# Optimization experiments

Measured on AMD Instinct MI355X. Metric: run time of the kernel, lower is better.

The kernel has to match this reference:

```python
import jax, jax.numpy as jnp
import numpy as np

N_RAYS, N_SAMPLES, GRID, APP_DIM, FEATC = 2048, 256, 128, 27, 128
VIEWPE, FEAPE = 2, 2
NEAR, FAR = 2.0, 6.0
AABB0, AABB1 = -1.5, 1.5
DENSITY_SHIFT, DISTANCE_SCALE = -10.0, 25.0
IN_MLPC = 2 * VIEWPE * 3 + 2 * FEAPE * APP_DIM + 3 + APP_DIM  # 150


def positional_encoding(x, freqs):
    fb = (2.0 ** jnp.arange(freqs)).astype(x.dtype)
    p = (x[..., None] * fb).reshape(x.shape[:-1] + (freqs * x.shape[-1],))
    return jnp.concatenate([jnp.sin(p), jnp.cos(p)], axis=-1)


def trilinear(vol, coords):
    # vol: [C, D, H, W]; coords: [P, 3] in [-1, 1] ordered (x, y, z) like torch grid_sample (align_corners=True)
    C, D, H, W = vol.shape
    x = (coords[:, 0] + 1.0) * 0.5 * (W - 1)
    y = (coords[:, 1] + 1.0) * 0.5 * (H - 1)
    z = (coords[:, 2] + 1.0) * 0.5 * (D - 1)
    x0 = jnp.clip(jnp.floor(x), 0, W - 2).astype(jnp.int32)
    y0 = jnp.clip(jnp.floor(y), 0, H - 2).astype(jnp.int32)
    z0 = jnp.clip(jnp.floor(z), 0, D - 2).astype(jnp.int32)
    x1, y1, z1 = x0 + 1, y0 + 1, z0 + 1
    fx, fy, fz = x - x0, y - y0, z - z0
    g = lambda zi, yi, xi: vol[:, zi, yi, xi]  # [C, P]
    out = (g(z0, y0, x0) * ((1 - fz) * (1 - fy) * (1 - fx))
           + g(z0, y0, x1) * ((1 - fz) * (1 - fy) * fx)
           + g(z0, y1, x0) * ((1 - fz) * fy * (1 - fx))
           + g(z0, y1, x1) * ((1 - fz) * fy * fx)
           + g(z1, y0, x0) * (fz * (1 - fy) * (1 - fx))
           + g(z1, y0, x1) * (fz * (1 - fy) * fx)
           + g(z1, y1, x0) * (fz * fy * (1 - fx))
           + g(z1, y1, x1) * (fz * fy * fx))
    return out  # [C, P]


def setup_inputs() -> dict:
    key = jax.random.key(0)
    ks = jax.random.split(key, 10)
    return {
        'rays_o': jax.random.uniform(ks[0], (N_RAYS, 3), jnp.float32, -0.5, 0.5) + jnp.array([0.0, 0.0, -4.0]),
        'rays_d': jax.random.normal(ks[1], (N_RAYS, 3), jnp.float32) * 0.1 + jnp.array([0.0, 0.0, 1.0]),
        'density_volume': jax.random.normal(ks[2], (1, GRID, GRID, GRID), jnp.float32) * 2.0 + 10.0,
        'app_volume': jax.random.normal(ks[3], (APP_DIM, GRID, GRID, GRID), jnp.float32) * 0.1,
        'w1': jax.random.normal(ks[4], (IN_MLPC, FEATC), jnp.float32) * 0.05,
        'b1': jnp.zeros((FEATC,), jnp.float32),
        'w2': jax.random.normal(ks[5], (FEATC, FEATC), jnp.float32) * 0.05,
        'b2': jnp.zeros((FEATC,), jnp.float32),
        'w3': jax.random.normal(ks[6], (FEATC, 3), jnp.float32) * 0.05,
        'b3': jnp.zeros((3,), jnp.float32),
    }


def reference(rays_o, rays_d, density_volume, app_volume, w1, b1, w2, b2, w3, b3):
    viewdirs = rays_d / jnp.linalg.norm(rays_d, axis=-1, keepdims=True)  # [N, 3]
    z_vals = jnp.linspace(NEAR, FAR, N_SAMPLES, dtype=rays_o.dtype)      # [S]
    z_vals = jnp.broadcast_to(z_vals, (N_RAYS, N_SAMPLES))
    pts = rays_o[:, None, :] + viewdirs[:, None, :] * z_vals[..., None]  # [N, S, 3]
    dists = jnp.concatenate([z_vals[:, 1:] - z_vals[:, :-1], z_vals[:, -1:] * 0 + (FAR - NEAR) / (N_SAMPLES - 1)], axis=-1)

    # normalize_coord: (xyz - aabb0) * (2 / aabbSize) - 1
    coords = jnp.clip((pts - AABB0) * (2.0 / (AABB1 - AABB0)) - 1.0, -1.0, 1.0).reshape(-1, 3)

    # density lookup + feature2density (softplus with shift)
    sigma_feat = trilinear(density_volume, coords)[0].reshape(N_RAYS, N_SAMPLES)
    sigma = jax.nn.softplus(sigma_feat + DENSITY_SHIFT)

    # raw2alpha: alpha, cumprod transmittance, weights
    alpha = 1.0 - jnp.exp(-sigma * dists * DISTANCE_SCALE)               # [N, S]
    T = jnp.cumprod(jnp.concatenate([jnp.ones((N_RAYS, 1), alpha.dtype), 1.0 - alpha + 1e-10], axis=-1), axis=-1)
    weights = alpha * T[:, :-1]                                          # [N, S]

    # MLPRender_Fea shading on all sampled points
    feat = trilinear(app_volume, coords).T                               # [P, app_dim]
    vd = jnp.broadcast_to(viewdirs[:, None, :], (N_RAYS, N_SAMPLES, 3)).reshape(-1, 3)
    mlp_in = jnp.concatenate([feat, vd, positional_encoding(feat, FEAPE), positional_encoding(vd, VIEWPE)], axis=-1)
    h = jax.nn.relu(mlp_in @ w1 + b1)
    h = jax.nn.relu(h @ w2 + b2)
    rgb = jax.nn.sigmoid(h @ w3 + b3).reshape(N_RAYS, N_SAMPLES, 3)

    acc_map = jnp.sum(weights, axis=-1)                                  # [N]
    rgb_map = jnp.sum(weights[..., None] * rgb, axis=-2)                 # [N, 3]
    rgb_map = jnp.clip(rgb_map + (1.0 - acc_map)[..., None], 0.0, 1.0)   # white background
    return rgb_map
```

## Files before the change

kernel.cpp:

```cpp
#include <hip/hip_runtime.h>
#include <math.h>
#include <limits.h>

#define N_RAYS 2048
#define NSAMP  256
#define NPTS   (N_RAYS * NSAMP)
#define NCHUNK (NPTS / 64)
#define GRIDN  128
#define G2     (GRIDN * GRIDN)
#define G3     (GRIDN * GRIDN * GRIDN)
#define APPC   27
#define CHP    28
#define FEATC  128
#define K1PAD  160
#define ASTR   168
#define HSTR   136
#define H2STR  130

typedef __attribute__((ext_vector_type(8))) short short8;
typedef __attribute__((ext_vector_type(4))) float float4v;

__device__ __forceinline__ unsigned short f2bf(float f) {
  unsigned int u = __float_as_uint(f);
  return (unsigned short)((u + 0x7FFFu + ((u >> 16) & 1u)) >> 16);
}
__device__ __forceinline__ float bf2f(unsigned short u) {
  return __uint_as_float(((unsigned int)u) << 16);
}

__device__ __forceinline__ void grid_coords(float cx, float cy, float cz,
                                            int& x0, int& y0, int& z0,
                                            float& fx, float& fy, float& fz) {
  float x = (cx + 1.0f) * 0.5f * 127.0f;
  float y = (cy + 1.0f) * 0.5f * 127.0f;
  float z = (cz + 1.0f) * 0.5f * 127.0f;
  float x0f = fminf(fmaxf(floorf(x), 0.0f), 126.0f);
  float y0f = fminf(fmaxf(floorf(y), 0.0f), 126.0f);
  float z0f = fminf(fmaxf(floorf(z), 0.0f), 126.0f);
  x0 = (int)x0f; y0 = (int)y0f; z0 = (int)z0f;
  fx = x - x0f; fy = y - y0f; fz = z - z0f;
}

__global__ __launch_bounds__(256)
void dvol_transpose(const float* __restrict__ dvol, float* __restrict__ dvolT) {
  __shared__ float tile[32][33];
  int y  = blockIdx.x & 127;
  int zt = ((blockIdx.x >> 7) & 3) * 32;
  int xt = (blockIdx.x >> 9) * 32;
  int tx = threadIdx.x & 31;
  int r0 = threadIdx.x >> 5;
  #pragma unroll
  for (int i = 0; i < 4; ++i) {
    int zr = r0 + i * 8;
    tile[zr][tx] = dvol[((zt + zr) * GRIDN + y) * GRIDN + xt + tx];
  }
  __syncthreads();
  #pragma unroll
  for (int i = 0; i < 4; ++i) {
    int xr = r0 + i * 8;
    dvolT[((xt + xr) * GRIDN + y) * GRIDN + zt + tx] = tile[tx][xr];
  }
}

template <bool TRANS>
__global__ __launch_bounds__(256)
void ray_kernel(const float* __restrict__ rays_o, const float* __restrict__ rays_d,
                const float* __restrict__ dvol,
                float* __restrict__ weights_ws, float* __restrict__ acc_ws,
                int* __restrict__ live_flags, int* __restrict__ block_bounds) {
  int r = blockIdx.x, s = threadIdx.x;
  int lane = s & 63, wv = s >> 6;
  float ox = rays_o[r*3+0], oy = rays_o[r*3+1], oz = rays_o[r*3+2];
  float dx = rays_d[r*3+0], dy = rays_d[r*3+1], dz = rays_d[r*3+2];
  float inv = rsqrtf(dx*dx + dy*dy + dz*dz);
  dx *= inv; dy *= inv; dz *= inv;
  float z = 2.0f + (4.0f / 255.0f) * (float)s;
  float px = ox + dx * z, py = oy + dy * z, pz = oz + dz * z;
  float cx = fminf(fmaxf((px + 1.5f) * (2.0f/3.0f) - 1.0f, -1.0f), 1.0f);
  float cy = fminf(fmaxf((py + 1.5f) * (2.0f/3.0f) - 1.0f, -1.0f), 1.0f);
  float cz = fminf(fmaxf((pz + 1.5f) * (2.0f/3.0f) - 1.0f, -1.0f), 1.0f);
  int x0, y0, z0; float fx, fy, fz;
  grid_coords(cx, cy, cz, x0, y0, z0, fx, fy, fz);
  float gx = 1.0f - fx, gy = 1.0f - fy, gz = 1.0f - fz;
  float sf;
  if (TRANS) {
    int base = (x0 * GRIDN + y0) * GRIDN + z0;
    float v000 = dvol[base],            v001 = dvol[base + 1];
    float v010 = dvol[base + GRIDN],    v011 = dvol[base + GRIDN + 1];
    float v100 = dvol[base + G2],       v101 = dvol[base + G2 + 1];
    float v110 = dvol[base + G2+GRIDN], v111 = dvol[base + G2+GRIDN+1];
    float c00 = gz * v000 + fz * v001;
    float c01 = gz * v010 + fz * v011;
    float c10 = gz * v100 + fz * v101;
    float c11 = gz * v110 + fz * v111;
    sf = gx * (gy * c00 + fy * c01) + fx * (gy * c10 + fy * c11);
  } else {
    int base = (z0 * GRIDN + y0) * GRIDN + x0;
    sf = dvol[base]            * (gz*gy*gx) + dvol[base + 1]            * (gz*gy*fx)
       + dvol[base + GRIDN]    * (gz*fy*gx) + dvol[base + GRIDN + 1]    * (gz*fy*fx)
       + dvol[base + G2]       * (fz*gy*gx) + dvol[base + G2 + 1]       * (fz*gy*fx)
       + dvol[base + G2+GRIDN] * (fz*fy*gx) + dvol[base + G2+GRIDN+1]   * (fz*fy*fx);
  }
  float xv = sf - 10.0f;
  float sp = fmaxf(xv, 0.0f) + __logf(1.0f + __expf(-fabsf(xv)));
  float alpha = 1.0f - __expf(-sp * (100.0f / 255.0f));

  float tt = 1.0f - alpha + 1e-10f;
  float p = tt;
  #pragma unroll
  for (int d = 1; d < 64; d <<= 1) {
    float v = __shfl_up(p, d);
    if (lane >= d) p *= v;
  }
  __shared__ float wtot[4], wacc[4];
  __shared__ int s_mn[4][3], s_mx[4][3], s_live[4];
  if (lane == 63) wtot[wv] = p;
  __syncthreads();
  float pref = 1.0f;
  #pragma unroll
  for (int w2i = 0; w2i < 3; ++w2i) if (w2i < wv) pref *= wtot[w2i];
  float ex = __shfl_up(p, 1);
  if (lane == 0) ex = 1.0f;
  float T = pref * ex;
  float wgt = alpha * T;
  weights_ws[r * NSAMP + s] = wgt;

  float sum = wgt;
  #pragma unroll
  for (int d = 32; d; d >>= 1) sum += __shfl_xor(sum, d);
  int xa = __shfl(x0, 0), xb = __shfl(x0, 63);
  int ya = __shfl(y0, 0), yb = __shfl(y0, 63);
  int za = __shfl(z0, 0), zb = __shfl(z0, 63);
  if (lane == 0) {
    wacc[wv] = sum;
    int live = (sum >= 1e-5f) ? 1 : 0;
    live_flags[r * 4 + wv] = live;
    s_live[wv] = live;
    s_mn[wv][0] = min(xa, xb); s_mx[wv][0] = max(xa, xb);
    s_mn[wv][1] = min(ya, yb); s_mx[wv][1] = max(ya, yb);
    s_mn[wv][2] = min(za, zb); s_mx[wv][2] = max(za, zb);
  }
  __syncthreads();
  if (s == 0) {
    acc_ws[r] = wacc[0] + wacc[1] + wacc[2] + wacc[3];
    int mn[3] = {INT_MAX, INT_MAX, INT_MAX};
    int mx[3] = {-1, -1, -1};
    #pragma unroll
    for (int w = 0; w < 4; ++w) {
      if (s_live[w]) {
        #pragma unroll
        for (int i = 0; i < 3; ++i) {
          mn[i] = min(mn[i], s_mn[w][i]);
          mx[i] = max(mx[i], s_mx[w][i]);
        }
      }
    }
    block_bounds[r*6+0] = mn[0]; block_bounds[r*6+1] = mn[1]; block_bounds[r*6+2] = mn[2];
    block_bounds[r*6+3] = mx[0] + 1; block_bounds[r*6+4] = mx[1] + 1; block_bounds[r*6+5] = mx[2] + 1;
  }
}

__global__ __launch_bounds__(256)
void compact_kernel(const int* __restrict__ live_flags, const int* __restrict__ block_bounds,
                    int* __restrict__ count, int* __restrict__ worklist,
                    int* __restrict__ bounds) {
  int t = threadIdx.x;
  int id = blockIdx.x * 256 + t;
  int lane = t & 63, wv = t >> 6;
  int flag = live_flags[id];
  unsigned long long m = __ballot(flag != 0);
  int prefix = __popcll(m & ((1ull << lane) - 1ull));
  int wcount = __popcll(m);
  __shared__ int wbase[4];
  if (lane == 0) wbase[wv] = wcount;
  __syncthreads();
  if (t == 0) {
    int tot = wbase[0] + wbase[1] + wbase[2] + wbase[3];
    int base = atomicAdd(count, tot);
    #pragma unroll
    for (int w = 0; w < 4; ++w) { int c = wbase[w]; wbase[w] = base; base += c; }
  }
  __syncthreads();
  if (flag) worklist[wbase[wv] + prefix] = id;

  if (t < 64) {
    int rr = blockIdx.x * 64 + t;
    int mn0 = block_bounds[rr*6+0], mn1 = block_bounds[rr*6+1], mn2 = block_bounds[rr*6+2];
    int mx0 = block_bounds[rr*6+3], mx1 = block_bounds[rr*6+4], mx2 = block_bounds[rr*6+5];
    #pragma unroll
    for (int d = 32; d; d >>= 1) {
      mn0 = min(mn0, __shfl_xor(mn0, d)); mx0 = max(mx0, __shfl_xor(mx0, d));
      mn1 = min(mn1, __shfl_xor(mn1, d)); mx1 = max(mx1, __shfl_xor(mx1, d));
      mn2 = min(mn2, __shfl_xor(mn2, d)); mx2 = max(mx2, __shfl_xor(mx2, d));
    }
    if (t == 0) {
      atomicMin(&bounds[0], mn0); atomicMax(&bounds[3], mx0);
      atomicMin(&bounds[1], mn1); atomicMax(&bounds[4], mx1);
      atomicMin(&bounds[2], mn2); atomicMax(&bounds[5], mx2);
    }
  }
}

__global__ __launch_bounds__(256)
void transpose_kernel(const float* __restrict__ avol, unsigned short* __restrict__ appT,
                      const int* __restrict__ bounds) {
  int vblk = blockIdx.x * 512;
  int zb = vblk >> 14;
  int yb = (vblk & 16383) >> 7;
  int zmin = bounds[2], zmax = bounds[5];
  int ymin = bounds[1], ymax = bounds[4];
  if (zb < zmin || zb > zmax) return;
  if (yb + 3 < ymin || yb > ymax) return;
  int v0 = vblk + threadIdx.x * 2;
  int y = (v0 & 16383) >> 7;
  int x = v0 & 127;
  if (y < ymin || y > ymax) return;
  int xmin = bounds[0], xmax = bounds[3];
  if (x + 1 < xmin || x > xmax) return;

  float2 v[APPC];
  #pragma unroll
  for (int c = 0; c < APPC; ++c) v[c] = *(const float2*)&avol[(size_t)c * G3 + v0];
  unsigned short* dst = appT + (size_t)v0 * CHP;
  #pragma unroll
  for (int i = 0; i < 7; ++i) {
    ushort4 o;
    o.x = f2bf(v[4*i+0].x); o.y = f2bf(v[4*i+1].x);
    o.z = (4*i+2 < APPC) ? f2bf(v[4*i+2].x) : (unsigned short)0;
    o.w = (4*i+3 < APPC) ? f2bf(v[4*i+3].x) : (unsigned short)0;
    *(ushort4*)&dst[4*i] = o;
  }
  #pragma unroll
  for (int i = 0; i < 7; ++i) {
    ushort4 o;
    o.x = f2bf(v[4*i+0].y); o.y = f2bf(v[4*i+1].y);
    o.z = (4*i+2 < APPC) ? f2bf(v[4*i+2].y) : (unsigned short)0;
    o.w = (4*i+3 < APPC) ? f2bf(v[4*i+3].y) : (unsigned short)0;
    *(ushort4*)&dst[CHP + 4*i] = o;
  }
}

__global__ __launch_bounds__(256)
void prep_weights(const float* __restrict__ w1, const float* __restrict__ w2,
                  unsigned short* __restrict__ w1T, unsigned short* __restrict__ w2T) {
  int t = blockIdx.x * 256 + threadIdx.x;
  if (t < 128 * K1PAD) {
    int n = t / K1PAD, k = t - n * K1PAD;
    w1T[t] = (k < 150) ? f2bf(w1[k * 128 + n]) : (unsigned short)0;
  } else {
    int i = t - 128 * K1PAD;
    if (i < 128 * 128) {
      int n = i >> 7, k = i & 127;
      w2T[i] = f2bf(w2[k * 128 + n]);
    }
  }
}

template <bool USET>
__global__ __launch_bounds__(256)
void shade_kernel(const float* __restrict__ rays_o, const float* __restrict__ rays_d,
                  const float* __restrict__ avol, const unsigned short* __restrict__ appT,
                  const unsigned short* __restrict__ w1T, const unsigned short* __restrict__ w2T,
                  const float* __restrict__ b1, const float* __restrict__ b2,
                  const float* __restrict__ w3, const float* __restrict__ b3,
                  const float* __restrict__ weights_ws, float* __restrict__ rgb_accum,
                  const int* __restrict__ count, int* __restrict__ work_ctr,
                  const int* __restrict__ worklist) {
  __shared__ unsigned short A_lds[64 * ASTR];
  __shared__ unsigned short h1_lds[64 * HSTR];
  __shared__ int s_idx, s_n;

  int t = threadIdx.x;
  int lane = t & 63, wv = t >> 6;

  if (t == 0) s_n = *count;

  for (;;) {
    __syncthreads();
    if (t == 0) s_idx = atomicAdd(work_ctr, 1);
    __syncthreads();
    if (s_idx >= s_n) break;
    int chunk = worklist[s_idx];
    int gp0 = chunk * 64;
    int r = gp0 >> 8;

    {
      int q = t & 3, pt = t >> 2;
      int gp = gp0 + pt, s = gp & 255;
      float ox = rays_o[r*3+0], oy = rays_o[r*3+1], oz = rays_o[r*3+2];
      float dx = rays_d[r*3+0], dy = rays_d[r*3+1], dz = rays_d[r*3+2];
      float inv = rsqrtf(dx*dx + dy*dy + dz*dz);
      dx *= inv; dy *= inv; dz *= inv;
      float z = 2.0f + (4.0f / 255.0f) * (float)s;
      float px = ox + dx * z, py = oy + dy * z, pz = oz + dz * z;
      float cx = fminf(fmaxf((px + 1.5f) * (2.0f/3.0f) - 1.0f, -1.0f), 1.0f);
      float cy = fminf(fmaxf((py + 1.5f) * (2.0f/3.0f) - 1.0f, -1.0f), 1.0f);
      float cz = fminf(fmaxf((pz + 1.5f) * (2.0f/3.0f) - 1.0f, -1.0f), 1.0f);
      int x0, y0, z0; float fxg, fyg, fzg;
      grid_coords(cx, cy, cz, x0, y0, z0, fxg, fyg, fzg);
      float gxg = 1.0f - fxg, gyg = 1.0f - fyg, gzg = 1.0f - fzg;
      float w8[8];
      w8[0] = gzg*gyg*gxg; w8[1] = gzg*gyg*fxg;
      w8[2] = gzg*fyg*gxg; w8[3] = gzg*fyg*fxg;
      w8[4] = fzg*gyg*gxg; w8[5] = fzg*gyg*fxg;
      w8[6] = fzg*fyg*gxg; w8[7] = fzg*fyg*fxg;
      int ibase = (z0 * GRIDN + y0) * GRIDN + x0;

      int vi = ibase + (q >> 1) * G2 + (q & 1) * GRIDN;
      float wA = w8[2*q], wB = w8[2*q+1];
      float part[27];
      if (USET) {
        const ushort4* c0 = (const ushort4*)(appT + (size_t)vi * CHP);
        const ushort4* c1 = (const ushort4*)(appT + (size_t)(vi + 1) * CHP);
        ushort4 a[7], b[7];
        #pragma unroll
        for (int i = 0; i < 7; ++i) { a[i] = c0[i]; b[i] = c1[i]; }
        #pragma unroll
        for (int c = 0; c < 27; ++c) {
          unsigned short ua = (&a[c >> 2].x)[c & 3];
          unsigned short ub = (&b[c >> 2].x)[c & 3];
          part[c] = wA * bf2f(ua) + wB * bf2f(ub);
        }
      } else {
        #pragma unroll
        for (int c = 0; c < 27; ++c) {
          const float* base = avol + (size_t)c * G3 + vi;
          part[c] = wA * base[0] + wB * base[1];
        }
      }
      #pragma unroll
      for (int c = 0; c < 27; ++c) {
        float v = part[c];
        v += __shfl_xor(v, 1);
        v += __shfl_xor(v, 2);
        part[c] = v;
      }
      float f[7];
      #pragma unroll
      for (int j = 0; j < 7; ++j) {
        float vlo = (q & 1) ? part[7 + j] : part[j];
        float vhi = (q & 1) ? part[(21 + j < 27) ? 21 + j : 26] : part[14 + j];
        f[j] = (q & 2) ? vhi : vlo;
      }
      unsigned short* Arow = A_lds + pt * ASTR;
      int cbase = 7 * q;
      #pragma unroll
      for (int j = 0; j < 7; ++j) {
        int c = cbase + j;
        if (c < 27) {
          float fv = f[j];
          Arow[c] = f2bf(fv);
          float s1 = __sinf(fv),      c1 = __cosf(fv);
          float s2 = __sinf(2.0f*fv), c2 = __cosf(2.0f*fv);
          Arow[30 + 2*c] = f2bf(s1); Arow[31 + 2*c] = f2bf(s2);
          Arow[84 + 2*c] = f2bf(c1); Arow[85 + 2*c] = f2bf(c2);
        }
      }
      if (q == 3) {
        float vd[3] = {dx, dy, dz};
        #pragma unroll
        for (int d = 0; d < 3; ++d) {
          Arow[27 + d] = f2bf(vd[d]);
          float s1 = __sinf(vd[d]),      c1 = __cosf(vd[d]);
          float s2 = __sinf(2.0f*vd[d]), c2 = __cosf(2.0f*vd[d]);
          Arow[138 + 2*d] = f2bf(s1); Arow[139 + 2*d] = f2bf(s2);
          Arow[144 + 2*d] = f2bf(c1); Arow[145 + 2*d] = f2bf(c2);
        }
      }
      if (q == 1) {
        #pragma unroll
        for (int i = 0; i < 5; ++i) *(unsigned int*)&Arow[150 + 2*i] = 0u;
      }
    }
    __syncthreads();

    int nlo = lane & 15;
    int koff = (lane >> 4) * 8;
    int mrow = wv * 16 + nlo;

    short8 a1[5];
    #pragma unroll
    for (int kt = 0; kt < 5; ++kt)
      a1[kt] = *(const short8*)&A_lds[mrow * ASTR + kt * 32 + koff];
    #pragma unroll
    for (int nt = 0; nt < 8; ++nt) {
      float4v acc = {0.f, 0.f, 0.f, 0.f};
      #pragma unroll
      for (int kt = 0; kt < 5; ++kt) {
        short8 b = *(const short8*)&w1T[(nt * 16 + nlo) * K1PAD + kt * 32 + koff];
        acc = __builtin_amdgcn_mfma_f32_16x16x32_bf16(a1[kt], b, acc, 0, 0, 0);
      }
      float bv = b1[nt * 16 + nlo];
      #pragma unroll
      for (int rg = 0; rg < 4; ++rg) {
        int m = wv * 16 + (lane >> 4) * 4 + rg;
        float hv = fmaxf(acc[rg] + bv, 0.0f);
        h1_lds[m * HSTR + nt * 16 + nlo] = f2bf(hv);
      }
    }
    __syncthreads();

    short8 a2[4];
    #pragma unroll
    for (int kt = 0; kt < 4; ++kt)
      a2[kt] = *(const short8*)&h1_lds[mrow * HSTR + kt * 32 + koff];
    unsigned short* h2 = A_lds;
    #pragma unroll
    for (int nt = 0; nt < 8; ++nt) {
      float4v acc = {0.f, 0.f, 0.f, 0.f};
      #pragma unroll
      for (int kt = 0; kt < 4; ++kt) {
        short8 b = *(const short8*)&w2T[(nt * 16 + nlo) * FEATC + kt * 32 + koff];
        acc = __builtin_amdgcn_mfma_f32_16x16x32_bf16(a2[kt], b, acc, 0, 0, 0);
      }
      float bv = b2[nt * 16 + nlo];
      #pragma unroll
      for (int rg = 0; rg < 4; ++rg) {
        int m = wv * 16 + (lane >> 4) * 4 + rg;
        float hv = fmaxf(acc[rg] + bv, 0.0f);
        h2[m * H2STR + nt * 16 + nlo] = f2bf(hv);
      }
    }
    __syncthreads();

    if (wv < 3) {
      int j = wv, pp = lane;
      const unsigned short* h2row = h2 + pp * H2STR;
      float sum = b3[j];
      #pragma unroll
      for (int k = 0; k < FEATC; k += 4) {
        ushort4 hv = *(const ushort4*)&h2row[k];
        sum += bf2f(hv.x) * w3[(k+0)*3 + j] + bf2f(hv.y) * w3[(k+1)*3 + j]
             + bf2f(hv.z) * w3[(k+2)*3 + j] + bf2f(hv.w) * w3[(k+3)*3 + j];
      }
      float val = (1.0f / (1.0f + __expf(-sum))) * weights_ws[gp0 + pp];
      #pragma unroll
      for (int d = 32; d; d >>= 1) val += __shfl_xor(val, d);
      if (pp == 0) atomicAdd(&rgb_accum[r * 3 + j], val);
    }
  }
}

__global__ void finish_kernel(const float* __restrict__ rgb_accum,
                              const float* __restrict__ acc_ws,
                              float* __restrict__ out) {
  int i = blockIdx.x * blockDim.x + threadIdx.x;
  if (i < N_RAYS * 3) {
    int r = i / 3;
    float v = rgb_accum[i] + 1.0f - acc_ws[r];
    out[i] = fminf(fmaxf(v, 0.0f), 1.0f);
  }
}

extern "C" void kernel_launch(void* const* d_in, const int* in_sizes, int n_in,
                              void* d_out, int out_size, void* d_ws, size_t ws_size,
                              hipStream_t stream) {
  const float* rays_o = (const float*)d_in[0];
  const float* rays_d = (const float*)d_in[1];
  const float* dvol   = (const float*)d_in[2];
  const float* avol   = (const float*)d_in[3];
  const float* w1     = (const float*)d_in[4];
  const float* b1     = (const float*)d_in[5];
  const float* w2     = (const float*)d_in[6];
  const float* b2     = (const float*)d_in[7];
  const float* w3     = (const float*)d_in[8];
  const float* b3     = (const float*)d_in[9];
  float* out = (float*)d_out;

  float* weights_ws = (float*)d_ws;
  float* acc_ws     = weights_ws + NPTS;
  float* rgb_accum  = acc_ws + N_RAYS;
  int*   count      = (int*)(rgb_accum + N_RAYS * 3);
  int*   work_ctr   = count + 1;
  int*   bounds     = work_ctr + 1;
  int*   worklist   = bounds + 6;
  int*   live_flags = worklist + NCHUNK;
  int*   block_bounds = live_flags + NCHUNK;
  unsigned short* w1T = (unsigned short*)(block_bounds + N_RAYS * 6);
  unsigned short* w2T = w1T + 128 * K1PAD;
  float* dvolT = (float*)(w2T + 128 * 128);
  unsigned short* appT = (unsigned short*)(dvolT + G3);

  size_t fixed_bytes = (size_t)(NPTS + N_RAYS + N_RAYS * 3 + 8 + 2 * NCHUNK + N_RAYS * 6) * 4
                     + (size_t)(128 * K1PAD + 128 * 128) * 2;
  bool usedt = ws_size >= fixed_bytes + (size_t)G3 * 4;
  bool uset  = ws_size >= fixed_bytes + (size_t)G3 * 4 + (size_t)G3 * CHP * 2;

  hipMemsetAsync(rgb_accum, 0, (N_RAYS * 3 + 2) * sizeof(float), stream);
  hipMemsetAsync(bounds, 0x7f, 3 * sizeof(int), stream);
  hipMemsetAsync(bounds + 3, 0, 3 * sizeof(int), stream);
  prep_weights<<<(128 * K1PAD + 128 * 128 + 255) / 256, 256, 0, stream>>>(w1, w2, w1T, w2T);
  if (usedt) {
    dvol_transpose<<<2048, 256, 0, stream>>>(dvol, dvolT);
    ray_kernel<true><<<N_RAYS, 256, 0, stream>>>(rays_o, rays_d, dvolT, weights_ws, acc_ws,
                                                 live_flags, block_bounds);
  } else {
    ray_kernel<false><<<N_RAYS, 256, 0, stream>>>(rays_o, rays_d, dvol, weights_ws, acc_ws,
                                                  live_flags, block_bounds);
  }
  compact_kernel<<<NCHUNK / 256, 256, 0, stream>>>(live_flags, block_bounds,
                                                   count, worklist, bounds);
  if (uset) {
    transpose_kernel<<<G3 / 512, 256, 0, stream>>>(avol, appT, bounds);
    shade_kernel<true><<<1024, 256, 0, stream>>>(rays_o, rays_d, avol, appT, w1T, w2T,
                                                 b1, b2, w3, b3, weights_ws, rgb_accum,
                                                 count, work_ctr, worklist);
  } else {
    shade_kernel<false><<<1024, 256, 0, stream>>>(rays_o, rays_d, avol, appT, w1T, w2T,
                                                  b1, b2, w3, b3, weights_ws, rgb_accum,
                                                  count, work_ctr, worklist);
  }
  finish_kernel<<<(N_RAYS * 3 + 255) / 256, 256, 0, stream>>>(rgb_accum, acc_ws, out);
}
```

Before: 466.8 us.

## Compact shading work per sample by weight threshold instead of per 64-sample chunk

Shading work is now compacted per sample rather than per 64-sample chunk. The ray kernel ballots samples whose weight exceeds a small threshold, and a single-block scan plus a scatter kernel build a dense list of live sample ids. The shade kernel then processes only those samples and writes per-point rgb without atomics, and the finish kernel reduces them per ray. This is meant to skip MLP work on negligible-weight samples inside live chunks, at the cost of extra launches, gather indirection and an approximation that drops contributions below the threshold.

```diff
diff --git a/kernel.cpp b/kernel.cpp
--- a/kernel.cpp
+++ b/kernel.cpp
@@ -5,7 +5,6 @@
 #define N_RAYS 2048
 #define NSAMP  256
 #define NPTS   (N_RAYS * NSAMP)
-#define NCHUNK (NPTS / 64)
 #define GRIDN  128
 #define G2     (GRIDN * GRIDN)
 #define G3     (GRIDN * GRIDN * GRIDN)
@@ -16,6 +15,7 @@
 #define ASTR   168
 #define HSTR   136
 #define H2STR  130
+#define WTH    1e-7f
 
 typedef __attribute__((ext_vector_type(8))) short short8;
 typedef __attribute__((ext_vector_type(4))) float float4v;
@@ -67,7 +67,8 @@
 void ray_kernel(const float* __restrict__ rays_o, const float* __restrict__ rays_d,
                 const float* __restrict__ dvol,
                 float* __restrict__ weights_ws, float* __restrict__ acc_ws,
-                int* __restrict__ live_flags, int* __restrict__ block_bounds) {
+                unsigned long long* __restrict__ ray_mask, int* __restrict__ ray_count,
+                int* __restrict__ block_bounds) {
   int r = blockIdx.x, s = threadIdx.x;
   int lane = s & 63, wv = s >> 6;
   float ox = rays_o[r*3+0], oy = rays_o[r*3+1], oz = rays_o[r*3+2];
@@ -113,7 +114,7 @@
     if (lane >= d) p *= v;
   }
   __shared__ float wtot[4], wacc[4];
-  __shared__ int s_mn[4][3], s_mx[4][3], s_live[4];
+  __shared__ int s_cnt[4], s_mn[4][3], s_mx[4][3], s_live[4];
   if (lane == 63) wtot[wv] = p;
   __syncthreads();
   float pref = 1.0f;
@@ -128,14 +129,16 @@
   float sum = wgt;
   #pragma unroll
   for (int d = 32; d; d >>= 1) sum += __shfl_xor(sum, d);
+
+  unsigned long long m = __ballot(wgt >= WTH);
   int xa = __shfl(x0, 0), xb = __shfl(x0, 63);
   int ya = __shfl(y0, 0), yb = __shfl(y0, 63);
   int za = __shfl(z0, 0), zb = __shfl(z0, 63);
   if (lane == 0) {
     wacc[wv] = sum;
-    int live = (sum >= 1e-5f) ? 1 : 0;
-    live_flags[r * 4 + wv] = live;
-    s_live[wv] = live;
+    ray_mask[r * 4 + wv] = m;
+    s_cnt[wv] = __popcll(m);
+    s_live[wv] = (m != 0ull) ? 1 : 0;
     s_mn[wv][0] = min(xa, xb); s_mx[wv][0] = max(xa, xb);
     s_mn[wv][1] = min(ya, yb); s_mx[wv][1] = max(ya, yb);
     s_mn[wv][2] = min(za, zb); s_mx[wv][2] = max(za, zb);
@@ -143,6 +146,7 @@
   __syncthreads();
   if (s == 0) {
     acc_ws[r] = wacc[0] + wacc[1] + wacc[2] + wacc[3];
+    ray_count[r] = s_cnt[0] + s_cnt[1] + s_cnt[2] + s_cnt[3];
     int mn[3] = {INT_MAX, INT_MAX, INT_MAX};
     int mx[3] = {-1, -1, -1};
     #pragma unroll
@@ -161,43 +165,77 @@
 }
 
 __global__ __launch_bounds__(256)
-void compact_kernel(const int* __restrict__ live_flags, const int* __restrict__ block_bounds,
-                    int* __restrict__ count, int* __restrict__ worklist,
-                    int* __restrict__ bounds) {
-  int t = threadIdx.x;
-  int id = blockIdx.x * 256 + t;
-  int lane = t & 63, wv = t >> 6;
-  int flag = live_flags[id];
-  unsigned long long m = __ballot(flag != 0);
-  int prefix = __popcll(m & ((1ull << lane) - 1ull));
-  int wcount = __popcll(m);
-  __shared__ int wbase[4];
-  if (lane == 0) wbase[wv] = wcount;
+void scan_kernel(const int* __restrict__ ray_count, const int* __restrict__ block_bounds,
+                 int* __restrict__ ray_base, int* __restrict__ count,
+                 int* __restrict__ work_ctr, int* __restrict__ bounds) {
+  int t = threadIdx.x, lane = t & 63, wv = t >> 6;
+  int c[8], tsum = 0;
+  #pragma unroll
+  for (int j = 0; j < 8; ++j) { c[j] = ray_count[t*8+j]; tsum += c[j]; }
+  int p = tsum;
+  #pragma unroll
+  for (int d = 1; d < 64; d <<= 1) { int v = __shfl_up(p, d); if (lane >= d) p += v; }
+  __shared__ int wsum[4];
+  if (lane == 63) wsum[wv] = p;
+  __syncthreads();
+  int pref = 0;
+  #pragma unroll
+  for (int w = 0; w < 3; ++w) if (w < wv) pref += wsum[w];
+  int excl = pref + p - tsum;
+  #pragma unroll
+  for (int j = 0; j < 8; ++j) { ray_base[t*8+j] = excl; excl += c[j]; }
+  if (t == 255) { count[0] = excl; work_ctr[0] = 0; }
+
+  int mn0 = INT_MAX, mn1 = INT_MAX, mn2 = INT_MAX, mx0 = -1, mx1 = -1, mx2 = -1;
+  #pragma unroll
+  for (int j = 0; j < 8; ++j) {
+    int r = t*8+j;
+    if (c[j] > 0) {
+      mn0 = min(mn0, block_bounds[r*6+0]); mx0 = max(mx0, block_bounds[r*6+3]);
+      mn1 = min(mn1, block_bounds[r*6+1]); mx1 = max(mx1, block_bounds[r*6+4]);
+      mn2 = min(mn2, block_bounds[r*6+2]); mx2 = max(mx2, block_bounds[r*6+5]);
+    }
+  }
+  #pragma unroll
+  for (int d = 32; d; d >>= 1) {
+    mn0 = min(mn0, __shfl_xor(mn0, d)); mx0 = max(mx0, __shfl_xor(mx0, d));
+    mn1 = min(mn1, __shfl_xor(mn1, d)); mx1 = max(mx1, __shfl_xor(mx1, d));
+    mn2 = min(mn2, __shfl_xor(mn2, d)); mx2 = max(mx2, __shfl_xor(mx2, d));
+  }
+  __shared__ int bmn[4][3], bmx[4][3];
+  if (lane == 0) {
+    bmn[wv][0] = mn0; bmn[wv][1] = mn1; bmn[wv][2] = mn2;
+    bmx[wv][0] = mx0; bmx[wv][1] = mx1; bmx[wv][2] = mx2;
+  }
   __syncthreads();
   if (t == 0) {
-    int tot = wbase[0] + wbase[1] + wbase[2] + wbase[3];
-    int base = atomicAdd(count, tot);
     #pragma unroll
-    for (int w = 0; w < 4; ++w) { int c = wbase[w]; wbase[w] = base; base += c; }
-  }
-  __syncthreads();
-  if (flag) worklist[wbase[wv] + prefix] = id;
-
-  if (t < 64) {
-    int rr = blockIdx.x * 64 + t;
-    int mn0 = block_bounds[rr*6+0], mn1 = block_bounds[rr*6+1], mn2 = block_bounds[rr*6+2];
-    int mx0 = block_bounds[rr*6+3], mx1 = block_bounds[rr*6+4], mx2 = block_bounds[rr*6+5];
-    #pragma unroll
-    for (int d = 32; d; d >>= 1) {
-      mn0 = min(mn0, __shfl_xor(mn0, d)); mx0 = max(mx0, __shfl_xor(mx0, d));
-      mn1 = min(mn1, __shfl_xor(mn1, d)); mx1 = max(mx1, __shfl_xor(mx1, d));
-      mn2 = min(mn2, __shfl_xor(mn2, d)); mx2 = max(mx2, __shfl_xor(mx2, d));
-    }
-    if (t == 0) {
-      atomicMin(&bounds[0], mn0); atomicMax(&bounds[3], mx0);
-      atomicMin(&bounds[1], mn1); atomicMax(&bounds[4], mx1);
-      atomicMin(&bounds[2], mn2); atomicMax(&bounds[5], mx2);
-    }
+    for (int w = 1; w < 4; ++w) {
+      #pragma unroll
+      for (int i = 0; i < 3; ++i) {
+        bmn[0][i] = min(bmn[0][i], bmn[w][i]);
+        bmx[0][i] = max(bmx[0][i], bmx[w][i]);
+      }
+    }
+    bounds[0] = bmn[0][0]; bounds[1] = bmn[0][1]; bounds[2] = bmn[0][2];
+    bounds[3] = bmx[0][0]; bounds[4] = bmx[0][1]; bounds[5] = bmx[0][2];
+  }
+}
+
+__global__ __launch_bounds__(256)
+void scatter_kernel(const unsigned long long* __restrict__ ray_mask,
+                    const int* __restrict__ ray_base, int* __restrict__ sample_list) {
+  int t = threadIdx.x, lane = t & 63, wv = t >> 6;
+  int r = blockIdx.x * 4 + wv;
+  int base = ray_base[r];
+  int off = 0;
+  #pragma unroll
+  for (int w = 0; w < 4; ++w) {
+    unsigned long long m = ray_mask[r * 4 + w];
+    int flag = (int)((m >> lane) & 1ull);
+    int pre = __popcll(m & ((1ull << lane) - 1ull));
+    if (flag) sample_list[base + off + pre] = r * 256 + w * 64 + lane;
+    off += __popcll(m);
   }
 }
 
@@ -263,30 +301,33 @@
                   const unsigned short* __restrict__ w1T, const unsigned short* __restrict__ w2T,
                   const float* __restrict__ b1, const float* __restrict__ b2,
                   const float* __restrict__ w3, const float* __restrict__ b3,
-                  const float* __restrict__ weights_ws, float* __restrict__ rgb_accum,
+                  const float* __restrict__ weights_ws, float* __restrict__ rgb_pts,
                   const int* __restrict__ count, int* __restrict__ work_ctr,
-                  const int* __restrict__ worklist) {
+                  const int* __restrict__ sample_list) {
   __shared__ unsigned short A_lds[64 * ASTR];
   __shared__ unsigned short h1_lds[64 * HSTR];
-  __shared__ int s_idx, s_n;
+  __shared__ float wlds[64];
+  __shared__ int s_idx, s_items, s_n;
 
   int t = threadIdx.x;
   int lane = t & 63, wv = t >> 6;
 
-  if (t == 0) s_n = *count;
+  if (t == 0) { s_n = *count; s_items = (s_n + 63) >> 6; }
 
   for (;;) {
     __syncthreads();
     if (t == 0) s_idx = atomicAdd(work_ctr, 1);
     __syncthreads();
-    if (s_idx >= s_n) break;
-    int chunk = worklist[s_idx];
-    int gp0 = chunk * 64;
-    int r = gp0 >> 8;
+    if (s_idx >= s_items) break;
+    int base64 = s_idx * 64;
+    int n = s_n;
 
     {
       int q = t & 3, pt = t >> 2;
-      int gp = gp0 + pt, s = gp & 255;
+      int i = base64 + pt;
+      int id = (i < n) ? sample_list[i] : -1;
+      int sid = max(id, 0);
+      int r = sid >> 8, s = sid & 255;
       float ox = rays_o[r*3+0], oy = rays_o[r*3+1], oz = rays_o[r*3+2];
       float dx = rays_d[r*3+0], dy = rays_d[r*3+1], dz = rays_d[r*3+2];
       float inv = rsqrtf(dx*dx + dy*dy + dz*dz);
@@ -306,6 +347,8 @@
       w8[6] = fzg*fyg*gxg; w8[7] = fzg*fyg*fxg;
       int ibase = (z0 * GRIDN + y0) * GRIDN + x0;
 
+      if (q == 0) wlds[pt] = (id >= 0) ? weights_ws[sid] : 0.0f;
+
       int vi = ibase + (q >> 1) * G2 + (q & 1) * GRIDN;
       float wA = w8[2*q], wB = w8[2*q+1];
       float part[27];
@@ -314,7 +357,7 @@
         const ushort4* c1 = (const ushort4*)(appT + (size_t)(vi + 1) * CHP);
         ushort4 a[7], b[7];
         #pragma unroll
-        for (int i = 0; i < 7; ++i) { a[i] = c0[i]; b[i] = c1[i]; }
+        for (int i2 = 0; i2 < 7; ++i2) { a[i2] = c0[i2]; b[i2] = c1[i2]; }
         #pragma unroll
         for (int c = 0; c < 27; ++c) {
           unsigned short ua = (&a[c >> 2].x)[c & 3];
@@ -324,8 +367,8 @@
       } else {
         #pragma unroll
         for (int c = 0; c < 27; ++c) {
-          const float* base = avol + (size_t)c * G3 + vi;
-          part[c] = wA * base[0] + wB * base[1];
+          const float* bptr = avol + (size_t)c * G3 + vi;
+          part[c] = wA * bptr[0] + wB * bptr[1];
         }
       }
       #pragma unroll
@@ -369,7 +412,7 @@
       }
       if (q == 1) {
         #pragma unroll
-        for (int i = 0; i < 5; ++i) *(unsigned int*)&Arow[150 + 2*i] = 0u;
+        for (int i2 = 0; i2 < 5; ++i2) *(unsigned int*)&Arow[150 + 2*i2] = 0u;
       }
     }
     __syncthreads();
@@ -433,22 +476,33 @@
         sum += bf2f(hv.x) * w3[(k+0)*3 + j] + bf2f(hv.y) * w3[(k+1)*3 + j]
              + bf2f(hv.z) * w3[(k+2)*3 + j] + bf2f(hv.w) * w3[(k+3)*3 + j];
       }
-      float val = (1.0f / (1.0f + __expf(-sum))) * weights_ws[gp0 + pp];
-      #pragma unroll
-      for (int d = 32; d; d >>= 1) val += __shfl_xor(val, d);
-      if (pp == 0) atomicAdd(&rgb_accum[r * 3 + j], val);
-    }
-  }
-}
-
-__global__ void finish_kernel(const float* __restrict__ rgb_accum,
-                              const float* __restrict__ acc_ws,
-                              float* __restrict__ out) {
-  int i = blockIdx.x * blockDim.x + threadIdx.x;
-  if (i < N_RAYS * 3) {
-    int r = i / 3;
-    float v = rgb_accum[i] + 1.0f - acc_ws[r];
-    out[i] = fminf(fmaxf(v, 0.0f), 1.0f);
+      float val = (1.0f / (1.0f + __expf(-sum))) * wlds[pp];
+      rgb_pts[(size_t)(base64 + pp) * 4 + j] = val;
+    }
+  }
+}
+
+__global__ __launch_bounds__(256)
+void finish_kernel(const float* __restrict__ rgb_pts, const int* __restrict__ ray_base,
+                   const int* __restrict__ ray_count, const float* __restrict__ acc_ws,
+                   float* __restrict__ out) {
+  int t = threadIdx.x, lane = t & 63, wv = t >> 6;
+  int r = blockIdx.x * 4 + wv;
+  int base = ray_base[r], cnt = ray_count[r];
+  float s0 = 0.f, s1 = 0.f, s2 = 0.f;
+  for (int i = lane; i < cnt; i += 64) {
+    const float4 v = *(const float4*)&rgb_pts[(size_t)(base + i) * 4];
+    s0 += v.x; s1 += v.y; s2 += v.z;
+  }
+  #pragma unroll
+  for (int d = 32; d; d >>= 1) {
+    s0 += __shfl_xor(s0, d); s1 += __shfl_xor(s1, d); s2 += __shfl_xor(s2, d);
+  }
+  if (lane == 0) {
+    float a = 1.0f - acc_ws[r];
+    out[r*3+0] = fminf(fmaxf(s0 + a, 0.0f), 1.0f);
+    out[r*3+1] = fminf(fmaxf(s1 + a, 0.0f), 1.0f);
+    out[r*3+2] = fminf(fmaxf(s2 + a, 0.0f), 1.0f);
   }
 }
 
@@ -469,46 +523,47 @@
 
   float* weights_ws = (float*)d_ws;
   float* acc_ws     = weights_ws + NPTS;
-  float* rgb_accum  = acc_ws + N_RAYS;
-  int*   count      = (int*)(rgb_accum + N_RAYS * 3);
+  float* rgb_pts    = acc_ws + N_RAYS;
+  int*   count      = (int*)(rgb_pts + (size_t)(NPTS + 64) * 4);
   int*   work_ctr   = count + 1;
   int*   bounds     = work_ctr + 1;
-  int*   worklist   = bounds + 6;
-  int*   live_flags = worklist + NCHUNK;
-  int*   block_bounds = live_flags + NCHUNK;
-  unsigned short* w1T = (unsigned short*)(block_bounds + N_RAYS * 6);
+  int*   ray_count  = bounds + 6;
+  int*   ray_base   = ray_count + N_RAYS;
+  int*   block_bounds = ray_base + N_RAYS;
+  int*   sample_list  = block_bounds + N_RAYS * 6;
+  unsigned long long* ray_mask = (unsigned long long*)(sample_list + NPTS + 64);
+  unsigned short* w1T = (unsigned short*)(ray_mask + N_RAYS * 4);
   unsigned short* w2T = w1T + 128 * K1PAD;
   float* dvolT = (float*)(w2T + 128 * 128);
   unsigned short* appT = (unsigned short*)(dvolT + G3);
 
-  size_t fixed_bytes = (size_t)(NPTS + N_RAYS + N_RAYS * 3 + 8 + 2 * NCHUNK + N_RAYS * 6) * 4
+  size_t fixed_bytes = ((size_t)NPTS + N_RAYS + (size_t)(NPTS + 64) * 4
+                        + 8 + 2 * N_RAYS + N_RAYS * 6 + NPTS + 64) * 4
+                     + (size_t)N_RAYS * 4 * 8
                      + (size_t)(128 * K1PAD + 128 * 128) * 2;
   bool usedt = ws_size >= fixed_bytes + (size_t)G3 * 4;
   bool uset  = ws_size >= fixed_bytes + (size_t)G3 * 4 + (size_t)G3 * CHP * 2;
 
-  hipMemsetAsync(rgb_accum, 0, (N_RAYS * 3 + 2) * sizeof(float), stream);
-  hipMemsetAsync(bounds, 0x7f, 3 * sizeof(int), stream);
-  hipMemsetAsync(bounds + 3, 0, 3 * sizeof(int), stream);
   prep_weights<<<(128 * K1PAD + 128 * 128 + 255) / 256, 256, 0, stream>>>(w1, w2, w1T, w2T);
   if (usedt) {
     dvol_transpose<<<2048, 256, 0, stream>>>(dvol, dvolT);
     ray_kernel<true><<<N_RAYS, 256, 0, stream>>>(rays_o, rays_d, dvolT, weights_ws, acc_ws,
-                                                 live_flags, block_bounds);
+                                                 ray_mask, ray_count, block_bounds);
   } else {
     ray_kernel<false><<<N_RAYS, 256, 0, stream>>>(rays_o, rays_d, dvol, weights_ws, acc_ws,
-                                                  live_flags, block_bounds);
-  }
-  compact_kernel<<<NCHUNK / 256, 256, 0, stream>>>(live_flags, block_bounds,
-                                                   count, worklist, bounds);
+                                                  ray_mask, ray_count, block_bounds);
+  }
+  scan_kernel<<<1, 256, 0, stream>>>(ray_count, block_bounds, ray_base, count, work_ctr, bounds);
+  scatter_kernel<<<N_RAYS / 4, 256, 0, stream>>>(ray_mask, ray_base, sample_list);
   if (uset) {
     transpose_kernel<<<G3 / 512, 256, 0, stream>>>(avol, appT, bounds);
     shade_kernel<true><<<1024, 256, 0, stream>>>(rays_o, rays_d, avol, appT, w1T, w2T,
-                                                 b1, b2, w3, b3, weights_ws, rgb_accum,
-                                                 count, work_ctr, worklist);
+                                                 b1, b2, w3, b3, weights_ws, rgb_pts,
+                                                 count, work_ctr, sample_list);
   } else {
     shade_kernel<false><<<1024, 256, 0, stream>>>(rays_o, rays_d, avol, appT, w1T, w2T,
-                                                  b1, b2, w3, b3, weights_ws, rgb_accum,
-                                                  count, work_ctr, worklist);
-  }
-  finish_kernel<<<(N_RAYS * 3 + 255) / 256, 256, 0, stream>>>(rgb_accum, acc_ws, out);
-}
+                                                  b1, b2, w3, b3, weights_ws, rgb_pts,
+                                                  count, work_ctr, sample_list);
+  }
+  finish_kernel<<<N_RAYS / 4, 256, 0, stream>>>(rgb_pts, ray_base, ray_count, acc_ws, out);
+}
```

Result: faster. 445.8 us (-4.5%).
